# Kernel tuning notes

Measured on AMD Instinct MI355X. Metric: run time of the kernel, lower is better.

## Reference

```python
import jax, jax.numpy as jnp
import numpy as np

B, N, D_MODEL, H = 2, 2048, 1024, 16
Q_CHUNK, K_CHUNK = 512, 1024
LN_EPS = 1e-5


def layer_norm(x, g, b):
    mu = x.mean(-1, keepdims=True)
    var = ((x - mu) ** 2).mean(-1, keepdims=True)
    return (x - mu) * jax.lax.rsqrt(var + LN_EPS) * g + b


def chunked_attention(q, k, v, qry_chunk, key_chunk):
    # q,k,v: [b,h,n,d]; memory-efficient chunked online-softmax attention
    b, h, n, d = q.shape
    q = q * (d ** -0.5)
    Q, K = n // qry_chunk, n // key_chunk
    qr = q.reshape(b, h, Q, qry_chunk, d)
    kr = k.reshape(b, h, K, key_chunk, d)
    vr = v.reshape(b, h, K, key_chunk, d)
    # per (q-chunk, k-chunk) scores: [b,h,Q,K,i,j]
    qk = jnp.einsum('bhqid,bhkjd->bhqkij', qr, kr)
    qk_max = jax.lax.stop_gradient(qk.max(axis=-1, keepdims=True))  # [b,h,Q,K,i,1]
    exp_qk = jnp.exp(qk - qk_max)
    attn = jnp.einsum('bhqkij,bhkjd->bhqkid', exp_qk, vr)
    exp_sum = exp_qk.sum(-1)            # [b,h,Q,K,i]
    m = qk_max[..., 0]                  # [b,h,Q,K,i]
    gmax = m.max(axis=3, keepdims=True)  # global max over key chunks
    renorm = jax.lax.stop_gradient(jnp.exp(m - gmax))
    num = (attn * renorm[..., None]).sum(axis=3)       # [b,h,Q,i,d]
    den = (exp_sum * renorm).sum(axis=3)[..., None]    # [b,h,Q,i,1]
    out = num / (1e-8 + den)
    return out.reshape(b, h, n, d)


def setup_inputs() -> dict:
    key = jax.random.key(0)
    ks = jax.random.split(key, 10)
    s = 0.02
    return {
        'x': jax.random.normal(ks[0], (B, N, D_MODEL), dtype=jnp.float32),
        'Wq': jax.random.normal(ks[1], (D_MODEL, D_MODEL), dtype=jnp.float32) * s,
        'bq': jnp.zeros((D_MODEL,), jnp.float32),
        'Wk': jax.random.normal(ks[2], (D_MODEL, D_MODEL), dtype=jnp.float32) * s,
        'bk': jnp.zeros((D_MODEL,), jnp.float32),
        'Wv': jax.random.normal(ks[3], (D_MODEL, D_MODEL), dtype=jnp.float32) * s,
        'bv': jnp.zeros((D_MODEL,), jnp.float32),
        'Wo': jax.random.normal(ks[4], (D_MODEL, D_MODEL), dtype=jnp.float32) * s,
        'bo': jnp.zeros((D_MODEL,), jnp.float32),
        'ln_g': jnp.ones((D_MODEL,), jnp.float32),
        'ln_b': jnp.zeros((D_MODEL,), jnp.float32),
    }


def reference(x, Wq, bq, Wk, bk, Wv, bv, Wo, bo, ln_g, ln_b):
    # qkv adapter: self-attention (key = val = qry = x)
    q = x @ Wq + bq
    k = x @ Wk + bk
    v = x @ Wv + bv
    # pre-norm on query path
    q = layer_norm(q, ln_g, ln_b)
    b, n, _ = q.shape
    d = D_MODEL // H
    qh = q.reshape(b, n, H, d).transpose(0, 2, 1, 3)
    kh = k.reshape(b, n, H, d).transpose(0, 2, 1, 3)
    vh = v.reshape(b, n, H, d).transpose(0, 2, 1, 3)
    attn = chunked_attention(qh, kh, vh, Q_CHUNK, K_CHUNK)
    out = attn.transpose(0, 2, 1, 3).reshape(b, n, D_MODEL)
    out = out + q  # residual with normed projected query
    return out @ Wo + bo
```

## Files before the change

kernel.cpp:

```cpp
#include <hip/hip_runtime.h>


typedef unsigned short u16;
typedef __attribute__((ext_vector_type(8))) short bf8v;
typedef __attribute__((ext_vector_type(4))) float f4v;

typedef __attribute__((address_space(1))) void gvoid;
typedef __attribute__((address_space(3))) void lvoid;
__device__ __forceinline__ void cp16(const void* g, void* l) {
  __builtin_amdgcn_global_load_lds((gvoid*)g, (lvoid*)l, 16, 0, 0);
}

__device__ __forceinline__ float bf2f(u16 u) {
  unsigned int x = ((unsigned int)u) << 16;
  float f; __builtin_memcpy(&f, &x, 4); return f;
}
__device__ __forceinline__ u16 f2bf(float f) {
  unsigned int x; __builtin_memcpy(&x, &f, 4);
  unsigned int r = (x + 0x7fffu + ((x >> 16) & 1u)) >> 16;
  return (u16)r;
}
__device__ __forceinline__ unsigned pack2bf(float a, float b) {
  unsigned ua, ub;
  __builtin_memcpy(&ua, &a, 4); __builtin_memcpy(&ub, &b, 4);
  return __builtin_amdgcn_perm(ub, ua, 0x07060302u);
}

#define KSCALE 0.18033688011f

__global__ void k_classify(const u16* a0, const u16* a1, const u16* a2, const u16* a3,
                           const u16* a4, const u16* a5, const u16* a6, const u16* a7,
                           const u16* a8, const u16* a9, const u16* a10, int* flags) {
  int t = threadIdx.x;
  if (t >= 11) return;
  const u16* arr[11] = {a0,a1,a2,a3,a4,a5,a6,a7,a8,a9,a10};
  const u16* p = arr[t];
  int ze = 0, no = 0, pe = 0;
  for (int i = 0; i < 128; ++i) {
    u16 he = p[2*i], ho = p[2*i+1];
    if (he == 0) ze++;
    if (ho != 0) no++;
    int e = (he >> 7) & 0xff;
    if (he == 0 || (e >= 64 && e <= 160)) pe++;
  }
  int isbf;
  if (ze >= 100 && no >= 64) isbf = 0;
  else isbf = (pe >= 100) ? 1 : 0;
  flags[t] = isbf;
}

__global__ __launch_bounds__(256) void k_convert_x(const void* xin, u16* xb, const int* flags) {
  size_t i = ((size_t)blockIdx.x * 256 + threadIdx.x) * 8;
  if (flags[0]) {
    *(float4*)(xb + i) = *((const float4*)((const u16*)xin + i));
  } else {
    const float* xf = (const float*)xin;
    float4 a = *(const float4*)(xf + i);
    float4 b = *(const float4*)(xf + i + 4);
    ushort4 o0, o1;
    o0.x = f2bf(a.x); o0.y = f2bf(a.y); o0.z = f2bf(a.z); o0.w = f2bf(a.w);
    o1.x = f2bf(b.x); o1.y = f2bf(b.y); o1.z = f2bf(b.z); o1.w = f2bf(b.w);
    *(ushort4*)(xb + i) = o0; *(ushort4*)(xb + i + 4) = o1;
  }
}

__global__ __launch_bounds__(256) void k_transpose_w(const void* W0, const void* W1,
    const void* W2, const void* W3, u16* wt, const int* flags) {
  __shared__ u16 tile[64 * 65];
  int z = blockIdx.z;
  const void* W = (z == 0) ? W0 : (z == 1) ? W1 : (z == 2) ? W2 : W3;
  int isb = flags[1 + 2*z];
  u16* dst = wt + (size_t)z * (1u << 20);
  int r0 = blockIdx.y * 64, c0 = blockIdx.x * 64;
  int t = threadIdx.x;
  for (int rr = 0; rr < 2; ++rr) {
    int row = rr * 32 + (t >> 3);
    int c8 = (t & 7) * 8;
    u16 v[8];
    if (isb) {
      const u16* Ws = (const u16*)W;
      ushort4 a = *(const ushort4*)&Ws[(size_t)(r0 + row) * 1024 + c0 + c8];
      ushort4 b = *(const ushort4*)&Ws[(size_t)(r0 + row) * 1024 + c0 + c8 + 4];
      v[0]=a.x; v[1]=a.y; v[2]=a.z; v[3]=a.w; v[4]=b.x; v[5]=b.y; v[6]=b.z; v[7]=b.w;
    } else {
      const float* Wf = (const float*)W;
      float4 a = *(const float4*)&Wf[(size_t)(r0 + row) * 1024 + c0 + c8];
      float4 b = *(const float4*)&Wf[(size_t)(r0 + row) * 1024 + c0 + c8 + 4];
      v[0]=f2bf(a.x); v[1]=f2bf(a.y); v[2]=f2bf(a.z); v[3]=f2bf(a.w);
      v[4]=f2bf(b.x); v[5]=f2bf(b.y); v[6]=f2bf(b.z); v[7]=f2bf(b.w);
    }
#pragma unroll
    for (int j = 0; j < 8; ++j) tile[row * 65 + c8 + j] = v[j];
  }
  __syncthreads();
  for (int rr = 0; rr < 2; ++rr) {
    int nrow = rr * 32 + (t >> 3);
    int k8 = (t & 7) * 8;
    u16 v[8];
#pragma unroll
    for (int j = 0; j < 8; ++j) v[j] = tile[(k8 + j) * 65 + nrow];
    ushort4 o0, o1;
    o0.x=v[0]; o0.y=v[1]; o0.z=v[2]; o0.w=v[3];
    o1.x=v[4]; o1.y=v[5]; o1.z=v[6]; o1.w=v[7];
    *(ushort4*)&dst[(size_t)(c0 + nrow) * 1024 + r0 + k8] = o0;
    *(ushort4*)&dst[(size_t)(c0 + nrow) * 1024 + r0 + k8 + 4] = o1;
  }
}

template <int MT>
__device__ __forceinline__ void gemm_bt(const u16* __restrict__ A, const u16* __restrict__ Bt,
    const void* __restrict__ bias, int bias_bf, void* __restrict__ Cout, int mode,
    float cscale) {
  constexpr int MI = MT / 32;
  __shared__ __align__(16) u16 As[2][MT * 32];
  __shared__ __align__(16) u16 Bs[2][128 * 32];
  const int tid = threadIdx.x;
  const int wave = tid >> 6, lane = tid & 63;
  const int qd = lane >> 4, ln = lane & 15;
  const int m0 = blockIdx.y * MT, n0 = blockIdx.x * 128;
  const int wr = (wave >> 1) * (MT / 2), wc = (wave & 1) * 64;
  const int r0 = wave * 16 + (lane >> 2);
  const int csrc = ((lane & 3) ^ ((lane >> 2) & 3)) * 8;
  const u16* Ag = &A[(size_t)m0 * 1024];
  const u16* Bg = &Bt[(size_t)n0 * 1024];
  const int co = (qd ^ (ln & 3)) * 8;
  f4v acc[MI][4];
#pragma unroll
  for (int i = 0; i < MI; ++i)
#pragma unroll
    for (int j = 0; j < 4; ++j) acc[i][j] = (f4v){0.f, 0.f, 0.f, 0.f};

#pragma unroll
  for (int t = 0; t < MT / 64; ++t)
    cp16(&Ag[(size_t)(t * 64 + r0) * 1024 + csrc], &As[0][(t * 256 + wave * 64) * 8]);
#pragma unroll
  for (int t = 0; t < 2; ++t)
    cp16(&Bg[(size_t)(t * 64 + r0) * 1024 + csrc], &Bs[0][(t * 256 + wave * 64) * 8]);

  for (int it = 0; it < 32; ++it) {
    __syncthreads();
    if (it < 31) {
      int ko = (it + 1) * 32;
      int bi = (it + 1) & 1;
#pragma unroll
      for (int t = 0; t < MT / 64; ++t)
        cp16(&Ag[(size_t)(t * 64 + r0) * 1024 + ko + csrc], &As[bi][(t * 256 + wave * 64) * 8]);
#pragma unroll
      for (int t = 0; t < 2; ++t)
        cp16(&Bg[(size_t)(t * 64 + r0) * 1024 + ko + csrc], &Bs[bi][(t * 256 + wave * 64) * 8]);
    }
    const u16* as = As[it & 1];
    const u16* bs = Bs[it & 1];
    bf8v af[MI], bfr[4];
#pragma unroll
    for (int i = 0; i < MI; ++i) af[i]  = *(const bf8v*)&as[(wr + i * 16 + ln) * 32 + co];
#pragma unroll
    for (int j = 0; j < 4; ++j) bfr[j] = *(const bf8v*)&bs[(wc + j * 16 + ln) * 32 + co];
#pragma unroll
    for (int i = 0; i < MI; ++i)
#pragma unroll
      for (int j = 0; j < 4; ++j)
        acc[i][j] = __builtin_amdgcn_mfma_f32_16x16x32_bf16(af[i], bfr[j], acc[i][j], 0, 0, 0);
  }
#pragma unroll
  for (int j = 0; j < 4; ++j) {
    int col = n0 + wc + j * 16 + ln;
    float bv = bias_bf ? bf2f(((const u16*)bias)[col]) : ((const float*)bias)[col];
#pragma unroll
    for (int i = 0; i < MI; ++i) {
      int row = m0 + wr + i * 16 + qd * 4;
      if (mode == 2) {
        ushort4 o4;
        o4.x = f2bf((acc[i][j][0] + bv) * cscale);
        o4.y = f2bf((acc[i][j][1] + bv) * cscale);
        o4.z = f2bf((acc[i][j][2] + bv) * cscale);
        o4.w = f2bf((acc[i][j][3] + bv) * cscale);
        int b_ = row >> 11, nl = row & 2047;
        int h_ = col >> 6, d6 = col & 63;
        int kt = nl >> 6, b0 = nl & 63;
        int c = b0 >> 5, g = (b0 >> 4) & 1, qd_f = (b0 >> 2) & 3;
        int dt = d6 >> 4, ln_f = d6 & 15;
        size_t off = (size_t)(b_ * 16 + h_) * 131072
                   + (size_t)(kt * 4096 + (c * 4 + dt) * 512 + (qd_f * 16 + ln_f) * 8 + g * 4);
        *(ushort4*)&((u16*)Cout)[off] = o4;
      } else {
#pragma unroll
        for (int r = 0; r < 4; ++r) {
          float v = (acc[i][j][r] + bv) * cscale;
          if (mode == 1) ((u16*)Cout)[(size_t)(row + r) * 1024 + col] = f2bf(v);
          else           ((float*)Cout)[(size_t)(row + r) * 1024 + col] = v;
        }
      }
    }
  }
}

__global__ __launch_bounds__(256) void k_gemm_qkv(const u16* xb, const u16* wt,
    const void* bq, const void* bk, const void* bv, const int* flags,
    u16* qpre, u16* kb, u16* vtb) {
  int z = blockIdx.z;
  const u16* Bt = wt + (size_t)z * (1u << 20);
  const void* bias = (z == 0) ? bq : (z == 1) ? bk : bv;
  if (z == 0)      gemm_bt<128>(xb, Bt, bias, flags[2], qpre, 1, 1.0f);
  else if (z == 1) gemm_bt<128>(xb, Bt, bias, flags[4], kb,   1, KSCALE);
  else             gemm_bt<128>(xb, Bt, bias, flags[6], vtb,  2, 1.0f);
}

__global__ __launch_bounds__(256) void k_gemm_out(const u16* A, const u16* Bt,
    const void* bias, const int* flags, void* out) {
  gemm_bt<64>(A, Bt, bias, flags[8], out, flags[0] ? 1 : 0, 1.0f);
}

__global__ __launch_bounds__(256) void k_layernorm(const u16* __restrict__ qp,
    const void* __restrict__ g, const void* __restrict__ bb, const int* flags,
    u16* __restrict__ out) {
  int row = blockIdx.x, t = threadIdx.x;
  const u16* rp = qp + (size_t)row * 1024;
  ushort4 u = *(const ushort4*)(rp + t * 4);
  float x0 = bf2f(u.x), x1 = bf2f(u.y), x2 = bf2f(u.z), x3 = bf2f(u.w);
  float s = x0 + x1 + x2 + x3;
  float s2 = x0 * x0 + x1 * x1 + x2 * x2 + x3 * x3;
  for (int off = 32; off; off >>= 1) { s += __shfl_down(s, off); s2 += __shfl_down(s2, off); }
  __shared__ float red[10];
  int wave = t >> 6, lane = t & 63;
  if (lane == 0) { red[wave] = s; red[4 + wave] = s2; }
  __syncthreads();
  if (t == 0) {
    float S = red[0] + red[1] + red[2] + red[3];
    float S2 = red[4] + red[5] + red[6] + red[7];
    float mu = S * (1.f / 1024.f);
    float var = S2 * (1.f / 1024.f) - mu * mu;
    red[8] = mu; red[9] = rsqrtf(var + 1e-5f);
  }
  __syncthreads();
  float mu = red[8], rstd = red[9];
  int gf = flags[9], bf = flags[10];
  int c = t * 4;
  float gv[4], bv[4];
#pragma unroll
  for (int k = 0; k < 4; ++k) {
    gv[k] = gf ? bf2f(((const u16*)g)[c + k]) : ((const float*)g)[c + k];
    bv[k] = bf ? bf2f(((const u16*)bb)[c + k]) : ((const float*)bb)[c + k];
  }
  ushort4 o;
  o.x = f2bf((x0 - mu) * rstd * gv[0] + bv[0]);
  o.y = f2bf((x1 - mu) * rstd * gv[1] + bv[1]);
  o.z = f2bf((x2 - mu) * rstd * gv[2] + bv[2]);
  o.w = f2bf((x3 - mu) * rstd * gv[3] + bv[3]);
  *(ushort4*)(out + (size_t)row * 1024 + c) = o;
}

__global__ __launch_bounds__(64) void k_attention(const u16* __restrict__ qln,
    const u16* __restrict__ kb, const u16* __restrict__ vfg, u16* __restrict__ attn) {
  const int x = blockIdx.x;
  const int xcd = x & 7, sl = x >> 3;
  const int bh = xcd * 4 + (sl >> 5), qt = sl & 31;
  const int b = bh >> 4, h = bh & 15;
  const int lane = threadIdx.x;
  const int qd = lane >> 4, ln = lane & 15;
  const int qrow0 = qt * 64;

  const u16* kgb = kb + (size_t)b * 2048 * 1024 + h * 64;
  const u16* vgb = vfg + (size_t)bh * 131072;

  bf8v qf[4][2];
#pragma unroll
  for (int qs = 0; qs < 4; ++qs) {
    const u16* qb = qln + ((size_t)b * 2048 + qrow0 + qs * 16 + ln) * 1024 + h * 64;
    qf[qs][0] = *(const bf8v*)(qb + qd * 8);
    qf[qs][1] = *(const bf8v*)(qb + 32 + qd * 8);
  }
  float ls[4][4];
  f4v o[4][4];
#pragma unroll
  for (int qs = 0; qs < 4; ++qs)
#pragma unroll
    for (int r = 0; r < 4; ++r) { ls[qs][r] = 0.f; o[qs][r] = (f4v){0.f, 0.f, 0.f, 0.f}; }

  for (int kt = 0; kt < 2048; kt += 64) {
    const u16* kr = kgb + (size_t)kt * 1024;
    bf8v kf[4][2];
#pragma unroll
    for (int ct = 0; ct < 4; ++ct) {
      kf[ct][0] = *(const bf8v*)(kr + (size_t)(ct * 16 + ln) * 1024 + qd * 8);
      kf[ct][1] = *(const bf8v*)(kr + (size_t)(ct * 16 + ln) * 1024 + 32 + qd * 8);
    }
    const u16* vr = vgb + (size_t)(kt >> 6) * 4096;
    bf8v vf[8];
#pragma unroll
    for (int cd = 0; cd < 8; ++cd)
      vf[cd] = *(const bf8v*)(vr + cd * 512 + lane * 8);

#pragma unroll
    for (int qs = 0; qs < 4; ++qs) {
      unsigned pk[4][2];
#pragma unroll
      for (int ct = 0; ct < 4; ++ct) {
        f4v z = (f4v){0.f, 0.f, 0.f, 0.f};
        z = __builtin_amdgcn_mfma_f32_16x16x32_bf16(kf[ct][0], qf[qs][0], z, 0, 0, 0);
        z = __builtin_amdgcn_mfma_f32_16x16x32_bf16(kf[ct][1], qf[qs][1], z, 0, 0, 0);
        float p0 = __builtin_amdgcn_exp2f(z[0]);
        float p1 = __builtin_amdgcn_exp2f(z[1]);
        float p2 = __builtin_amdgcn_exp2f(z[2]);
        float p3 = __builtin_amdgcn_exp2f(z[3]);
        ls[qs][0] += p0; ls[qs][1] += p1; ls[qs][2] += p2; ls[qs][3] += p3;
        pk[ct][0] = pack2bf(p0, p1);
        pk[ct][1] = pack2bf(p2, p3);
      }
#pragma unroll
      for (int c = 0; c < 2; ++c) {
        unsigned avals[4] = {pk[2*c][0], pk[2*c][1], pk[2*c+1][0], pk[2*c+1][1]};
        bf8v af; __builtin_memcpy(&af, avals, 16);
#pragma unroll
        for (int dt = 0; dt < 4; ++dt)
          o[qs][dt] = __builtin_amdgcn_mfma_f32_16x16x32_bf16(af, vf[c * 4 + dt], o[qs][dt], 0, 0, 0);
      }
    }
  }
#pragma unroll
  for (int qs = 0; qs < 4; ++qs) {
    float lsum = (ls[qs][0] + ls[qs][1]) + (ls[qs][2] + ls[qs][3]);
    lsum += __shfl_xor(lsum, 16);
    lsum += __shfl_xor(lsum, 32);
    float rden[4];
#pragma unroll
    for (int r = 0; r < 4; ++r) {
      float dv = __shfl(lsum, (lane & 48) + qd * 4 + r);
      rden[r] = __builtin_amdgcn_rcpf(1e-8f + dv);
    }
#pragma unroll
    for (int dt = 0; dt < 4; ++dt) {
#pragma unroll
      for (int r = 0; r < 4; ++r) {
        size_t idx = ((size_t)b * 2048 + qrow0 + qs * 16 + qd * 4 + r) * 1024
                   + h * 64 + dt * 16 + ln;
        float val = o[qs][dt][r] * rden[r] + bf2f(qln[idx]);
        attn[idx] = f2bf(val);
      }
    }
  }
}

extern "C" void kernel_launch(void* const* d_in, const int* in_sizes, int n_in,
                              void* d_out, int out_size, void* d_ws, size_t ws_size,
                              hipStream_t stream) {
  int* flags = (int*)d_ws;
  u16* base = (u16*)((char*)d_ws + 256);
  const size_t M1 = 1u << 20;
  u16* xb   = base;
  u16* wt   = base + 4 * M1;
  u16* qpre = base + 8 * M1;
  u16* kb   = base + 12 * M1;
  u16* vtb  = base + 16 * M1;
  u16* qln = xb;
  u16* at  = qpre;

  k_classify<<<1, 64, 0, stream>>>(
      (const u16*)d_in[0], (const u16*)d_in[1], (const u16*)d_in[2], (const u16*)d_in[3],
      (const u16*)d_in[4], (const u16*)d_in[5], (const u16*)d_in[6], (const u16*)d_in[7],
      (const u16*)d_in[8], (const u16*)d_in[9], (const u16*)d_in[10], flags);

  k_convert_x<<<2048, 256, 0, stream>>>(d_in[0], xb, flags);
  k_transpose_w<<<dim3(16, 16, 4), 256, 0, stream>>>(d_in[1], d_in[3], d_in[5], d_in[7], wt, flags);
  k_gemm_qkv<<<dim3(8, 32, 3), 256, 0, stream>>>(xb, wt, d_in[2], d_in[4], d_in[6], flags,
                                                 qpre, kb, vtb);
  k_layernorm<<<4096, 256, 0, stream>>>(qpre, d_in[9], d_in[10], flags, qln);
  k_attention<<<1024, 64, 0, stream>>>(qln, kb, vtb, at);
  k_gemm_out<<<dim3(8, 64), 256, 0, stream>>>(at, wt + 3 * M1, d_in[8], flags, d_out);
}
```

Before: 229.5 us.

## Split attention key range across four waves with LDS reduction

Each attention block now runs four waves instead of one, and each wave handles a quarter of the key sequence (512 keys) for the same 64 query rows. The partial outputs and row sums go through shared memory, and wave 0 reduces them, normalizes, adds the residual and stores. The aim is more parallelism and latency hiding in the attention kernel, which had only 1024 single-wave blocks. In exchange it adds about 50KB of LDS per block, a barrier, and a serial reduction on one wave. Summing unnormalized exponentials across waves stays correct only because the code uses no running-max rescaling.

```diff
diff --git a/kernel.cpp b/kernel.cpp
--- a/kernel.cpp
+++ b/kernel.cpp
@@ -250,15 +250,16 @@
   *(ushort4*)(out + (size_t)row * 1024 + c) = o;
 }
 
-__global__ __launch_bounds__(64) void k_attention(const u16* __restrict__ qln,
+__global__ __launch_bounds__(256) void k_attention(const u16* __restrict__ qln,
     const u16* __restrict__ kb, const u16* __restrict__ vfg, u16* __restrict__ attn) {
   const int x = blockIdx.x;
   const int xcd = x & 7, sl = x >> 3;
   const int bh = xcd * 4 + (sl >> 5), qt = sl & 31;
   const int b = bh >> 4, h = bh & 15;
-  const int lane = threadIdx.x;
+  const int tid = threadIdx.x, wave = tid >> 6, lane = tid & 63;
   const int qd = lane >> 4, ln = lane & 15;
   const int qrow0 = qt * 64;
+  __shared__ __align__(16) float xbuf[3][64 * 65];
 
   const u16* kgb = kb + (size_t)b * 2048 * 1024 + h * 64;
   const u16* vgb = vfg + (size_t)bh * 131072;
@@ -277,7 +278,8 @@
 #pragma unroll
     for (int r = 0; r < 4; ++r) { ls[qs][r] = 0.f; o[qs][r] = (f4v){0.f, 0.f, 0.f, 0.f}; }
 
-  for (int kt = 0; kt < 2048; kt += 64) {
+  const int kt0 = wave * 512;
+  for (int kt = kt0; kt < kt0 + 512; kt += 64) {
     const u16* kr = kgb + (size_t)kt * 1024;
     bf8v kf[4][2];
 #pragma unroll
@@ -317,25 +319,50 @@
       }
     }
   }
+  float dq[4];
 #pragma unroll
   for (int qs = 0; qs < 4; ++qs) {
     float lsum = (ls[qs][0] + ls[qs][1]) + (ls[qs][2] + ls[qs][3]);
     lsum += __shfl_xor(lsum, 16);
     lsum += __shfl_xor(lsum, 32);
-    float rden[4];
-#pragma unroll
-    for (int r = 0; r < 4; ++r) {
-      float dv = __shfl(lsum, (lane & 48) + qd * 4 + r);
-      rden[r] = __builtin_amdgcn_rcpf(1e-8f + dv);
-    }
-#pragma unroll
-    for (int dt = 0; dt < 4; ++dt) {
+    dq[qs] = lsum;
+  }
+  if (wave > 0) {
+    float* xb = xbuf[wave - 1];
+#pragma unroll
+    for (int qs = 0; qs < 4; ++qs) {
+#pragma unroll
+      for (int dt = 0; dt < 4; ++dt)
+#pragma unroll
+        for (int r = 0; r < 4; ++r)
+          xb[(qs * 16 + qd * 4 + r) * 65 + dt * 16 + ln] = o[qs][dt][r];
+      if (qd == 0) xb[(qs * 16 + ln) * 65 + 64] = dq[qs];
+    }
+  }
+  __syncthreads();
+  if (wave == 0) {
+#pragma unroll
+    for (int qs = 0; qs < 4; ++qs) {
+      float dtot = dq[qs] + xbuf[0][(qs * 16 + ln) * 65 + 64]
+                 + xbuf[1][(qs * 16 + ln) * 65 + 64]
+                 + xbuf[2][(qs * 16 + ln) * 65 + 64];
+      float rden[4];
 #pragma unroll
       for (int r = 0; r < 4; ++r) {
-        size_t idx = ((size_t)b * 2048 + qrow0 + qs * 16 + qd * 4 + r) * 1024
-                   + h * 64 + dt * 16 + ln;
-        float val = o[qs][dt][r] * rden[r] + bf2f(qln[idx]);
-        attn[idx] = f2bf(val);
+        float dv = __shfl(dtot, (lane & 48) + qd * 4 + r);
+        rden[r] = __builtin_amdgcn_rcpf(1e-8f + dv);
+      }
+#pragma unroll
+      for (int dt = 0; dt < 4; ++dt) {
+#pragma unroll
+        for (int r = 0; r < 4; ++r) {
+          int q6 = qs * 16 + qd * 4 + r, d6 = dt * 16 + ln;
+          float sum = o[qs][dt][r] + xbuf[0][q6 * 65 + d6]
+                    + xbuf[1][q6 * 65 + d6] + xbuf[2][q6 * 65 + d6];
+          size_t idx = ((size_t)b * 2048 + qrow0 + q6) * 1024 + h * 64 + d6;
+          float val = sum * rden[r] + bf2f(qln[idx]);
+          attn[idx] = f2bf(val);
+        }
       }
     }
   }
@@ -365,6 +392,6 @@
   k_gemm_qkv<<<dim3(8, 32, 3), 256, 0, stream>>>(xb, wt, d_in[2], d_in[4], d_in[6], flags,
                                                  qpre, kb, vtb);
   k_layernorm<<<4096, 256, 0, stream>>>(qpre, d_in[9], d_in[10], flags, qln);
-  k_attention<<<1024, 64, 0, stream>>>(qln, kb, vtb, at);
+  k_attention<<<1024, 256, 0, stream>>>(qln, kb, vtb, at);
   k_gemm_out<<<dim3(8, 64), 256, 0, stream>>>(at, wt + 3 * M1, d_in[8], flags, d_out);
 }
```

Result: slower. 250.9 us (+9.3%).
